# Kernel optimization log

Hardware: AMD Instinct MI355X
Metric: run time of the kernel (lower is better)

## Reference

```python
import jax, jax.numpy as jnp
import numpy as np

NBINS = (128, 64, 32)   # knots per stacked transform
N_GENES = 5000
N_ELEM = 4_000_000


def _split_parameters(unnormalized):
    # mirror of QuadraticSplineStack._split_parameters: [heights(n), widths(n-1)] per transform
    splits = []
    for n in NBINS:
        splits += [n, n - 1]
    parts = jnp.split(unnormalized, np.cumsum(splits)[:-1].tolist(), axis=-1)
    return list(zip(parts[0::2], parts[1::2]))


def _bin_search(table, gix, x):
    # vectorized per-element binary search: searchsorted(table[gix], x, side='right') - 1,
    # clamped to valid bin range [0, K-2]. table: [G, K] sorted; gix, x: [N].
    K = table.shape[-1]
    lo = jnp.zeros(x.shape, jnp.int32)
    hi = jnp.full(x.shape, K, jnp.int32)
    for _ in range(int(np.ceil(np.log2(K + 1)))):
        mid = jnp.clip((lo + hi) // 2, 0, K - 1)
        pred = table[gix, mid] <= x
        lo = jnp.where(pred, mid + 1, lo)
        hi = jnp.where(pred, hi, mid)
    return jnp.clip(lo - 1, 0, K - 2)


def _quadratic_spline_forward(x, gix, unnorm_heights, unnorm_widths):
    # per-gene tables
    widths = jax.nn.softmax(unnorm_widths, axis=-1)                      # [G, n-1]
    locs = jnp.cumsum(widths, axis=-1)
    locs = jnp.pad(locs.at[:, -1].set(1.0), ((0, 0), (1, 0)))            # [G, n] bin_locations
    eh = jnp.exp(unnorm_heights)                                         # [G, n]
    area = jnp.sum(0.5 * (eh[:, :-1] + eh[:, 1:]) * widths, axis=-1, keepdims=True)
    heights = eh / area                                                  # pdf knot heights, integrates to 1
    cdf = jnp.cumsum(0.5 * (heights[:, :-1] + heights[:, 1:]) * widths, axis=-1)
    left_cdf = jnp.pad(cdf.at[:, -1].set(1.0), ((0, 0), (1, 0)))         # [G, n] bin_left_cdf

    # locate bin per element, then gather scalar coefficients
    b = _bin_search(locs, gix, x)                                        # [N] in [0, n-2]
    w = widths[gix, b]
    lh = heights[gix, b]
    rh = heights[gix, b + 1]
    bl = locs[gix, b]
    lc = left_cdf[gix, b]

    alpha = (x - bl) / w
    out = (0.5 * (rh - lh) * w) * alpha * alpha + (lh * w) * alpha + lc
    out = jnp.clip(out, 0.0, 1.0)
    logabsdet = jnp.log(alpha * (rh - lh) + lh)
    return out, logabsdet


def setup_inputs() -> dict:
    key = jax.random.key(0)
    k1, k2, k3 = jax.random.split(key, 3)
    x = jax.random.uniform(k1, (N_ELEM,), dtype=jnp.float32, minval=1e-4, maxval=1.0 - 1e-4)
    local_gene_ix = jax.random.randint(k2, (N_ELEM,), 0, N_GENES)
    total = sum(n + (n - 1) for n in NBINS)  # 445
    unnormalized = jax.random.normal(k3, (N_GENES, total), dtype=jnp.float32) * 0.1
    return {"x": x, "local_gene_ix": local_gene_ix, "unnormalized": unnormalized}


def reference(x, local_gene_ix, unnormalized):
    gix = local_gene_ix.astype(jnp.int32)
    outputs = x
    logabsdet = jnp.zeros_like(x)
    for uh, uw in _split_parameters(unnormalized):
        outputs, lad = _quadratic_spline_forward(outputs, gix, uh, uw)
        logabsdet = logabsdet + lad
    return outputs, logabsdet
```

## Files before the change

kernel.cpp:

```cpp
#include <hip/hip_runtime.h>
#include <hip/hip_bf16.h>
#include <hip/hip_fp16.h>

#define N_GENES_MAX 5000
#define PARAMS_PER_GENE 445

__device__ uint2 g_k0[(size_t)N_GENES_MAX * 128];
__device__ uint2 g_k1[(size_t)N_GENES_MAX * 64];
__device__ uint2 g_k2[(size_t)N_GENES_MAX * 32];

static __device__ __forceinline__ unsigned f2h(float f) {
    union { __half h; unsigned short u; } c;
    c.h = __float2half_rn(f);
    return (unsigned)c.u;
}
static __device__ __forceinline__ float h2f(unsigned u) {
    union { unsigned short u; __half h; } c;
    c.u = (unsigned short)u;
    return __half2float(c.h);
}

static __device__ __forceinline__ float wscan_incl(float v) {
    const int lane = threadIdx.x & 63;
    #pragma unroll
    for (int off = 1; off < 64; off <<= 1) {
        float u = __shfl_up(v, off, 64);
        if (lane >= off) v += u;
    }
    return v;
}
static __device__ __forceinline__ float wmax64(float v) {
    #pragma unroll
    for (int off = 32; off > 0; off >>= 1) v = fmaxf(v, __shfl_xor(v, off, 64));
    return v;
}
static __device__ __forceinline__ float wsum64(float v) {
    #pragma unroll
    for (int off = 32; off > 0; off >>= 1) v += __shfl_xor(v, off, 64);
    return v;
}

__global__ void build_knots(const float* __restrict__ params) {
    const int g = blockIdx.x;
    const int t = blockIdx.y;
    const int ns[3]   = {128, 64, 32};
    const int poff[3] = {0, 255, 382};

    const int n = ns[t];
    const int m = n - 1;
    const float* ph = params + (size_t)g * PARAMS_PER_GENE + poff[t];
    const float* pw = ph + n;

    __shared__ float s2[2];
    __shared__ float s_scan[128];
    __shared__ float s_h[129];
    __shared__ float s_loc[128];
    __shared__ float s_cdf[128];

    const int tid  = threadIdx.x;
    const int lane = tid & 63;
    const int wv   = tid >> 6;

    const float uw = (tid < m) ? pw[tid] : -1e30f;
    float vmax = wmax64(uw);
    if (lane == 0) s2[wv] = vmax;
    __syncthreads();
    const float mx = fmaxf(s2[0], s2[1]);
    __syncthreads();

    const float e = (tid < m) ? __expf(uw - mx) : 0.0f;

    float sc = wscan_incl(e);
    if (lane == 63) s2[wv] = sc;
    __syncthreads();
    if (wv == 1) sc += s2[0];
    s_scan[tid] = sc;
    __syncthreads();

    const float S = s_scan[m - 1];
    const float invS = 1.0f / S;
    if (tid == 0) s_loc[0] = 0.0f;
    if (tid < m) s_loc[tid + 1] = (tid == m - 1) ? 1.0f : s_scan[tid] * invS;
    const float w_i = e * invS;

    const float eh = (tid < n) ? __expf(ph[tid]) : 0.0f;
    s_h[tid] = eh;
    if (tid == 0) s_h[128] = 0.0f;
    __syncthreads();

    const float term = (tid < m) ? 0.5f * (s_h[tid] + s_h[tid + 1]) * w_i : 0.0f;
    float ts = wsum64(term);
    if (lane == 0) s2[wv] = ts;
    __syncthreads();
    const float area = s2[0] + s2[1];
    __syncthreads();

    const float ia = 1.0f / area;
    const float hgt = eh * ia;

    float c = wscan_incl(term * ia);
    if (lane == 63) s2[wv] = c;
    __syncthreads();
    if (wv == 1) c += s2[0];
    s_scan[tid] = c;
    __syncthreads();

    if (tid == 0) s_cdf[0] = 0.0f;
    if (tid < m) s_cdf[tid + 1] = (tid == m - 1) ? 1.0f : s_scan[tid];
    __syncthreads();

    if (tid < n) {
        const float loc = s_loc[tid];
        uint2 kt;
        kt.x = __float_as_uint(loc);
        kt.y = (f2h(hgt) << 16) | f2h(s_cdf[tid] - loc);
        if (t == 0)      g_k0[(size_t)g * 128 + tid] = kt;
        else if (t == 1) g_k1[(size_t)g * 64 + tid] = kt;
        else             g_k2[(size_t)g * 32 + tid] = kt;
    }
}

template <int K>
static __device__ __forceinline__ void stage(const uint2* __restrict__ kn,
                                             float& x, float& lad) {
    int b = (int)(x * (float)(K - 1));
    b = (b < 0) ? 0 : ((b > K - 2) ? K - 2 : b);
    uint2 k0 = kn[b];
    uint2 k1 = kn[b + 1];
    float l0 = __uint_as_float(k0.x);
    float l1 = __uint_as_float(k1.x);
    while (b > 0 && l0 > x) {
        --b;
        k1 = k0; l1 = l0;
        k0 = kn[b]; l0 = __uint_as_float(k0.x);
    }
    while (b < K - 2 && l1 <= x) {
        ++b;
        k0 = k1; l0 = l1;
        k1 = kn[b + 1]; l1 = __uint_as_float(k1.x);
    }
    const float lh = h2f(k0.y >> 16);
    const float rh = h2f(k1.y >> 16);
    const float lc = l0 + h2f(k0.y & 0xffffu);
    const float w  = l1 - l0;
    const float alpha = (x - l0) / w;
    float o = (0.5f * (rh - lh) * w) * alpha * alpha + (lh * w) * alpha + lc;
    o = fminf(fmaxf(o, 0.0f), 1.0f);
    lad += __logf(alpha * (rh - lh) + lh);
    x = o;
}

static __device__ __forceinline__ void eval_one(float& x, int g, float& lad) {
    stage<128>(g_k0 + (size_t)g * 128, x, lad);
    stage<64> (g_k1 + (size_t)g * 64,  x, lad);
    stage<32> (g_k2 + (size_t)g * 32,  x, lad);
}

typedef float fvec2 __attribute__((ext_vector_type(2)));
typedef int   ivec2 __attribute__((ext_vector_type(2)));

__global__ void spline_eval(const float* __restrict__ x_in,
                            const int* __restrict__ gix,
                            float* __restrict__ out, int N) {
    const int i = blockIdx.x * blockDim.x + threadIdx.x;
    const int i2 = i * 2;
    if (i2 + 1 < N) {
        const fvec2 xv = __builtin_nontemporal_load((const fvec2*)(x_in + i2));
        const ivec2 gv = __builtin_nontemporal_load((const ivec2*)(gix + i2));
        float x0 = xv.x, x1 = xv.y;
        float l0 = 0.0f, l1 = 0.0f;
        eval_one(x0, gv.x, l0);
        eval_one(x1, gv.y, l1);
        fvec2 o0; o0.x = x0; o0.y = x1;
        fvec2 o1; o1.x = l0; o1.y = l1;
        __builtin_nontemporal_store(o0, (fvec2*)(out + i2));
        __builtin_nontemporal_store(o1, (fvec2*)(out + N + i2));
    } else if (i2 < N) {
        float x0 = x_in[i2];
        float l0 = 0.0f;
        eval_one(x0, gix[i2], l0);
        out[i2] = x0;
        out[N + i2] = l0;
    }
}

extern "C" void kernel_launch(void* const* d_in, const int* in_sizes, int n_in,
                              void* d_out, int out_size, void* d_ws, size_t ws_size,
                              hipStream_t stream) {
    const float* x      = (const float*)d_in[0];
    const int*   gix    = (const int*)d_in[1];
    const float* params = (const float*)d_in[2];
    float* out = (float*)d_out;

    const int N = in_sizes[0];
    const int G = in_sizes[2] / PARAMS_PER_GENE;

    build_knots<<<dim3(G, 3), 128, 0, stream>>>(params);

    const int block = 256;
    const int nh = (N + 1) / 2;
    spline_eval<<<(nh + block - 1) / block, block, 0, stream>>>(x, gix, out, N);
}
```

Baseline: 206.6 us.

## Split spline evaluation into two kernels with an intermediate buffer

Splits the fused three-stage evaluation into two kernels. The first runs the 128-knot stage and writes x, the gene index and the partial log-det (as fp16) to a global intermediate. The second reads that buffer and runs the 64- and 32-knot stages. The aim is to shrink each kernel's working set of knot tables so gathers hit cache better. In exchange it adds an extra 32 MB global round trip, loses precision by storing the partial log-det in fp16, and packing the gene index in 16 bits caps the gene count at 65536.

Result: faster. 189.7 us (-8.2%).

```diff
diff --git a/kernel.cpp b/kernel.cpp
--- a/kernel.cpp
+++ b/kernel.cpp
@@ -3,11 +3,13 @@
 #include <hip/hip_fp16.h>
 
 #define N_GENES_MAX 5000
+#define N_ELEM_MAX  4000000
 #define PARAMS_PER_GENE 445
 
 __device__ uint2 g_k0[(size_t)N_GENES_MAX * 128];
 __device__ uint2 g_k1[(size_t)N_GENES_MAX * 64];
 __device__ uint2 g_k2[(size_t)N_GENES_MAX * 32];
+__device__ uint2 g_mid[N_ELEM_MAX];
 
 static __device__ __forceinline__ unsigned f2h(float f) {
     union { __half h; unsigned short u; } c;
@@ -150,18 +152,12 @@
     x = o;
 }
 
-static __device__ __forceinline__ void eval_one(float& x, int g, float& lad) {
-    stage<128>(g_k0 + (size_t)g * 128, x, lad);
-    stage<64> (g_k1 + (size_t)g * 64,  x, lad);
-    stage<32> (g_k2 + (size_t)g * 32,  x, lad);
-}
-
 typedef float fvec2 __attribute__((ext_vector_type(2)));
 typedef int   ivec2 __attribute__((ext_vector_type(2)));
-
-__global__ void spline_eval(const float* __restrict__ x_in,
-                            const int* __restrict__ gix,
-                            float* __restrict__ out, int N) {
+typedef unsigned uvec4 __attribute__((ext_vector_type(4)));
+
+__global__ void spline_evalA(const float* __restrict__ x_in,
+                             const int* __restrict__ gix, int N) {
     const int i = blockIdx.x * blockDim.x + threadIdx.x;
     const int i2 = i * 2;
     if (i2 + 1 < N) {
@@ -169,16 +165,52 @@
         const ivec2 gv = __builtin_nontemporal_load((const ivec2*)(gix + i2));
         float x0 = xv.x, x1 = xv.y;
         float l0 = 0.0f, l1 = 0.0f;
-        eval_one(x0, gv.x, l0);
-        eval_one(x1, gv.y, l1);
+        stage<128>(g_k0 + (size_t)gv.x * 128, x0, l0);
+        stage<128>(g_k0 + (size_t)gv.y * 128, x1, l1);
+        uvec4 mid;
+        mid.x = __float_as_uint(x0);
+        mid.y = ((unsigned)gv.x << 16) | f2h(l0);
+        mid.z = __float_as_uint(x1);
+        mid.w = ((unsigned)gv.y << 16) | f2h(l1);
+        __builtin_nontemporal_store(mid, (uvec4*)(g_mid + i2));
+    } else if (i2 < N) {
+        float x0 = x_in[i2];
+        float l0 = 0.0f;
+        const int g = gix[i2];
+        stage<128>(g_k0 + (size_t)g * 128, x0, l0);
+        uint2 m;
+        m.x = __float_as_uint(x0);
+        m.y = ((unsigned)g << 16) | f2h(l0);
+        g_mid[i2] = m;
+    }
+}
+
+__global__ void spline_evalB(float* __restrict__ out, int N) {
+    const int i = blockIdx.x * blockDim.x + threadIdx.x;
+    const int i2 = i * 2;
+    if (i2 + 1 < N) {
+        const uvec4 mid = __builtin_nontemporal_load((const uvec4*)(g_mid + i2));
+        float x0 = __uint_as_float(mid.x);
+        float x1 = __uint_as_float(mid.z);
+        const int g0 = (int)(mid.y >> 16);
+        const int g1 = (int)(mid.w >> 16);
+        float l0 = h2f(mid.y & 0xffffu);
+        float l1 = h2f(mid.w & 0xffffu);
+        stage<64>(g_k1 + (size_t)g0 * 64, x0, l0);
+        stage<64>(g_k1 + (size_t)g1 * 64, x1, l1);
+        stage<32>(g_k2 + (size_t)g0 * 32, x0, l0);
+        stage<32>(g_k2 + (size_t)g1 * 32, x1, l1);
         fvec2 o0; o0.x = x0; o0.y = x1;
         fvec2 o1; o1.x = l0; o1.y = l1;
         __builtin_nontemporal_store(o0, (fvec2*)(out + i2));
         __builtin_nontemporal_store(o1, (fvec2*)(out + N + i2));
     } else if (i2 < N) {
-        float x0 = x_in[i2];
-        float l0 = 0.0f;
-        eval_one(x0, gix[i2], l0);
+        const uint2 mid = g_mid[i2];
+        float x0 = __uint_as_float(mid.x);
+        const int g0 = (int)(mid.y >> 16);
+        float l0 = h2f(mid.y & 0xffffu);
+        stage<64>(g_k1 + (size_t)g0 * 64, x0, l0);
+        stage<32>(g_k2 + (size_t)g0 * 32, x0, l0);
         out[i2] = x0;
         out[N + i2] = l0;
     }
@@ -199,5 +231,7 @@
 
     const int block = 256;
     const int nh = (N + 1) / 2;
-    spline_eval<<<(nh + block - 1) / block, block, 0, stream>>>(x, gix, out, N);
-}
+    const int grid = (nh + block - 1) / block;
+    spline_evalA<<<grid, block, 0, stream>>>(x, gix, N);
+    spline_evalB<<<grid, block, 0, stream>>>(out, N);
+}
```
